# Kernel optimization log

Measured on AMD Instinct MI355X. Metric: run time of the kernel, lower is better.

## Reference

```python
import jax, jax.numpy as jnp
import numpy as np

# Static config (Swin-T stage 1, SW-MSA)
B = 32; H = 56; W = 56; C = 96; NH = 3; WS = 7; SHIFT = 3
N = WS * WS                 # tokens per window (49)
NW = (H // WS) * (W // WS)  # windows per image (64)
HD = C // NH                # head dim (32)
SCALE = HD ** -0.5
EPS = 1e-3  # keras LayerNormalization default epsilon


def _rel_index():
    # Matches tf.stack(tf.meshgrid(h, w)) with default 'xy' indexing
    xx, yy = np.meshgrid(np.arange(WS), np.arange(WS))
    coords = np.stack([xx, yy]).reshape(2, -1)              # [2, 49]
    rel = (coords[:, :, None] - coords[:, None, :]).transpose(1, 2, 0)
    rel[:, :, 0] += WS - 1
    rel[:, :, 1] += WS - 1
    rel[:, :, 0] *= 2 * WS - 1
    return rel.sum(-1)                                       # [49, 49]

REL_IDX = jnp.asarray(_rel_index())


def _attn_mask():
    # Standard Swin shifted-window attention mask
    img = np.zeros((H, W))
    cnt = 0
    sl = (slice(0, -WS), slice(-WS, -SHIFT), slice(-SHIFT, None))
    for hs in sl:
        for ws_ in sl:
            img[hs, ws_] = cnt
            cnt += 1
    win = img.reshape(H // WS, WS, W // WS, WS).transpose(0, 2, 1, 3).reshape(-1, N)
    diff = win[:, None, :] - win[:, :, None]
    return jnp.asarray(np.where(diff != 0, -100.0, 0.0), dtype=np.float32)  # [nW,49,49]

MASK = _attn_mask()


def _ln(x, g, b):
    mu = x.mean(-1, keepdims=True)
    var = ((x - mu) ** 2).mean(-1, keepdims=True)
    return (x - mu) / jnp.sqrt(var + EPS) * g + b


def setup_inputs() -> dict:
    key = jax.random.key(0)
    ks = jax.random.split(key, 6)
    f32 = jnp.float32
    return {
        "x": jax.random.normal(ks[0], (B, H * W, C), f32),
        "norm1_g": jnp.ones((C,), f32), "norm1_b": jnp.zeros((C,), f32),
        "qkv_w": jax.random.normal(ks[1], (C, 3 * C), f32) * 0.02,
        "qkv_b": jnp.zeros((3 * C,), f32),
        "bias_table": jax.random.normal(ks[2], ((2 * WS - 1) ** 2, NH), f32) * 0.02,
        "proj_w": jax.random.normal(ks[3], (C, C), f32) * 0.02,
        "proj_b": jnp.zeros((C,), f32),
        "norm2_g": jnp.ones((C,), f32), "norm2_b": jnp.zeros((C,), f32),
        "fc1_w": jax.random.normal(ks[4], (C, 4 * C), f32) * 0.02,
        "fc1_b": jnp.zeros((4 * C,), f32),
        "fc2_w": jax.random.normal(ks[5], (4 * C, C), f32) * 0.02,
        "fc2_b": jnp.zeros((C,), f32),
    }


def reference(x, norm1_g, norm1_b, qkv_w, qkv_b, bias_table, proj_w, proj_b,
              norm2_g, norm2_b, fc1_w, fc1_b, fc2_w, fc2_b):
    shortcut = x
    h = _ln(x, norm1_g, norm1_b).reshape(B, H, W, C)
    # cyclic shift (SW-MSA)
    h = jnp.roll(h, (-SHIFT, -SHIFT), axis=(1, 2))
    # window partition -> [B*nW, N, C]
    h = h.reshape(B, H // WS, WS, W // WS, WS, C).transpose(0, 1, 3, 2, 4, 5).reshape(-1, N, C)
    qkv = (h @ qkv_w + qkv_b).reshape(-1, N, 3, NH, HD).transpose(2, 0, 3, 1, 4)
    q, k, v = qkv[0], qkv[1], qkv[2]            # each [B*nW, NH, N, HD]
    attn = jnp.einsum('bhnd,bhmd->bhnm', q * SCALE, k)
    bias = bias_table[REL_IDX.reshape(-1)].reshape(N, N, NH).transpose(2, 0, 1)
    attn = attn + bias[None]
    attn = attn.reshape(B, NW, NH, N, N) + MASK[None, :, None]
    attn = attn.reshape(-1, NH, N, N)
    # NOTE: source applies softmax twice (once in branch, once unconditionally)
    attn = jax.nn.softmax(jax.nn.softmax(attn, axis=-1), axis=-1)
    o = jnp.einsum('bhnm,bhmd->bhnd', attn, v).transpose(0, 2, 1, 3).reshape(-1, N, C)
    o = o @ proj_w + proj_b
    # window reverse + reverse cyclic shift
    o = o.reshape(B, H // WS, W // WS, WS, WS, C).transpose(0, 1, 3, 2, 4, 5).reshape(B, H, W, C)
    o = jnp.roll(o, (SHIFT, SHIFT), axis=(1, 2)).reshape(B, H * W, C)
    x = shortcut + o
    y = _ln(x, norm2_g, norm2_b)
    # NOTE: source Mlp applies gelu in Dense activation AND again in call -> double gelu
    y = jax.nn.gelu(y @ fc1_w + fc1_b, approximate=False)
    y = jax.nn.gelu(y, approximate=False)
    y = y @ fc2_w + fc2_b
    return x + y
```

## Files before the change

kernel.cpp:

```cpp
#include <hip/hip_runtime.h>
#include <math.h>

#define BB   32
#define HH   56
#define WWI  56
#define CC   96
#define NHD  3
#define WSZ  7
#define SHF  3
#define NTK  49
#define NWIN 64
#define HDM  32
#define TOT  (BB*HH*WWI)
#define QKSCALE 0.17677669529663687f
#define LEPS 1e-3f

typedef __attribute__((ext_vector_type(8))) short s8v;
typedef __attribute__((ext_vector_type(4))) float fx4;
typedef unsigned long long ull_t;

#define MFMA16(a,b,c) __builtin_amdgcn_mfma_f32_16x16x32_bf16((a),(b),(c),0,0,0)

__device__ __forceinline__ unsigned short f2bf(float f) {
    union { float f; unsigned u; } v; v.f = f;
    unsigned r = v.u + 0x7FFFu + ((v.u >> 16) & 1u);
    return (unsigned short)(r >> 16);
}

__device__ __forceinline__ float gelu_t(float x) {
    float x2 = x * x;
#if __has_builtin(__builtin_amdgcn_exp2f)
    float z = x * fmaf(-0.10294326f, x2, -2.3022082f);
    float e = __builtin_amdgcn_exp2f(z);
#else
    float z = x * fmaf(-0.07135529f, x2, -1.5957691f);
    float e = __expf(z);
#endif
    return x * __builtin_amdgcn_rcpf(1.f + e);
}

__device__ __forceinline__ int wtok_to_orig(int wt) {
    int win = wt / NTK;
    int p   = wt - win * NTK;
    int b   = win >> 6;
    int w   = win & 63;
    int wi = w >> 3, wj = w & 7;
    int pi = p / WSZ, pj = p - pi * WSZ;
    int r = wi * WSZ + pi + SHF; if (r >= HH) r -= HH;
    int c = wj * WSZ + pj + SHF; if (c >= WWI) c -= WWI;
    return b * (HH * WWI) + r * WWI + c;
}

__device__ __forceinline__ void ln_frag(const float* __restrict__ row,
                                        const float* __restrict__ gg,
                                        const float* __restrict__ bb,
                                        int g4, s8v ha[3])
{
    float h[24];
    #pragma unroll
    for (int ks = 0; ks < 3; ++ks) {
        fx4 v0 = *reinterpret_cast<const fx4*>(row + ks * 32 + g4 * 8);
        fx4 v1 = *reinterpret_cast<const fx4*>(row + ks * 32 + g4 * 8 + 4);
        h[ks*8+0]=v0.x; h[ks*8+1]=v0.y; h[ks*8+2]=v0.z; h[ks*8+3]=v0.w;
        h[ks*8+4]=v1.x; h[ks*8+5]=v1.y; h[ks*8+6]=v1.z; h[ks*8+7]=v1.w;
    }
    float s = 0.f, s2 = 0.f;
    #pragma unroll
    for (int j = 0; j < 24; ++j) { s += h[j]; s2 = fmaf(h[j], h[j], s2); }
    s  += __shfl_xor(s, 16);  s  += __shfl_xor(s, 32);
    s2 += __shfl_xor(s2, 16); s2 += __shfl_xor(s2, 32);
    const float mu = s * (1.f/CC);
    const float rs = rsqrtf(s2 * (1.f/CC) - mu * mu + LEPS);
    #pragma unroll
    for (int ks = 0; ks < 3; ++ks) {
        union { s8v v; unsigned short u[8]; } p;
        #pragma unroll
        for (int j = 0; j < 8; ++j) {
            int c = ks * 32 + g4 * 8 + j;
            p.u[j] = f2bf((h[ks*8+j] - mu) * rs * gg[c] + bb[c]);
        }
        ha[ks] = p.v;
    }
}

extern "C" __global__ void p0_prep(const float* __restrict__ qw, const float* __restrict__ pw,
                                   const float* __restrict__ w1, const float* __restrict__ w2,
                                   const float* __restrict__ btab,
                                   unsigned short* __restrict__ wsw)
{
    int i = blockIdx.x * 256 + threadIdx.x;
    if (i < 27648) {
        int e = i & 7, f = i >> 3;
        int lane = f & 63, fid = f >> 6;
        int ks = fid % 3, t = fid / 3;
        int nt = t % 6, ck = t / 6;
        int n = ck * 96 + nt * 16 + (lane & 15);
        int k = ks * 32 + (lane >> 4) * 8 + e;
        float v = qw[k * 288 + n];
        if (n < 96) v *= QKSCALE;
        wsw[i] = f2bf(v);
    } else if (i < 36864) {
        int j = i - 27648;
        int e = j & 7, f = j >> 3;
        int lane = f & 63, fid = f >> 6;
        int ks = fid % 3, nt = fid / 3;
        int n = nt * 16 + (lane & 15);
        int k = ks * 32 + (lane >> 4) * 8 + e;
        wsw[i] = f2bf(pw[k * 96 + n]);
    } else if (i < 73728) {
        int j = i - 36864;
        int e = j & 7, f = j >> 3;
        int lane = f & 63, fid = f >> 6;
        int ks = fid % 3, t = fid / 3;
        int nt = t & 3, ck = t >> 2;
        int n = ck * 64 + nt * 16 + (lane & 15);
        int k = ks * 32 + (lane >> 4) * 8 + e;
        wsw[i] = f2bf(w1[k * 384 + n]);
    } else if (i < 110592) {
        int j = i - 73728;
        int e = j & 7, f = j >> 3;
        int lane = f & 63, fid = f >> 6;
        int ks = fid & 1, t = fid >> 1;
        int nt = t % 6, ck = t / 6;
        int n = nt * 16 + (lane & 15);
        int k = ck * 64 + ks * 32 + (lane >> 4) * 8 + e;
        wsw[i] = f2bf(w2[k * 96 + n]);
    } else if (i < 159744) {
        float* bmf = (float*)(wsw + 110592);
        int j = i - 110592;
        int r = j & 3, lane = (j >> 2) & 63;
        int fid = j >> 8;
        int mtnt = fid & 15, t = fid >> 4;
        int mt = mtnt >> 2, nt = mtnt & 3;
        int hd = t % 3, cls = t / 3;
        int m = mt * 16 + (lane >> 4) * 4 + r; if (m > 48) m = 48;
        int n = nt * 16 + (lane & 15);
        float val = 0.f;
        if (n < 49) {
            int it = m / 7, jt = m - it * 7;
            int iu = n / 7, ju = n - iu * 7;
            int li  = (cls & 2) ? (it < 4 ? 1 : 2) : 0;
            int lj  = (cls & 1) ? (jt < 4 ? 1 : 2) : 0;
            int lui = (cls & 2) ? (iu < 4 ? 1 : 2) : 0;
            int luj = (cls & 1) ? (ju < 4 ? 1 : 2) : 0;
            int bidx = (jt - ju + 6) * 13 + (it - iu + 6);
            val = btab[bidx * 3 + hd] + ((li*3+lj) == (lui*3+luj) ? 0.f : -100.f);
        }
        bmf[j] = val;
    }
}

#define LDQ 104
extern "C" __global__ void __launch_bounds__(256, 2) k12_fused(
    const float* __restrict__ x, const float* __restrict__ g1, const float* __restrict__ b1,
    const unsigned short* __restrict__ qwtf, const float* __restrict__ qb,
    const float* __restrict__ bmf, unsigned short* __restrict__ ovb)
{
    __shared__ unsigned short Qs[64 * LDQ];
    __shared__ unsigned short Ks[64 * LDQ];
    __shared__ unsigned short P[3][64 * 72];
    const int tid = threadIdx.x, wave = tid >> 6, lane = tid & 63;
    const int l15 = lane & 15, g4 = lane >> 4;
    const int win = blockIdx.x;
    const int g0  = win * NTK;

    s8v ha[3];
    {
        int row = wave * 16 + l15;
        int tok = row > 48 ? 48 : row;
        ln_frag(x + (size_t)wtok_to_orig(g0 + tok) * CC, g1, b1, g4, ha);
    }

    #pragma unroll
    for (int ck = 0; ck < 3; ++ck) {
        fx4 acc[6];
        #pragma unroll
        for (int nt = 0; nt < 6; ++nt) acc[nt] = (fx4){0.f,0.f,0.f,0.f};
        #pragma unroll
        for (int ks = 0; ks < 3; ++ks) {
            #pragma unroll
            for (int nt = 0; nt < 6; ++nt) {
                s8v b = *reinterpret_cast<const s8v*>(
                    &qwtf[(((ck * 6 + nt) * 3 + ks) * 64 + lane) * 8]);
                acc[nt] = MFMA16(ha[ks], b, acc[nt]);
            }
        }
        const int rowb = wave * 16 + g4 * 4;
        if (ck == 0) {
            #pragma unroll
            for (int nt = 0; nt < 6; ++nt) {
                const int col = nt * 16 + l15;
                const float qbc = qb[col] * QKSCALE;
                #pragma unroll
                for (int r = 0; r < 4; ++r)
                    Qs[(rowb + r) * LDQ + col] = f2bf(acc[nt][r] + qbc);
            }
        } else if (ck == 1) {
            #pragma unroll
            for (int nt = 0; nt < 6; ++nt) {
                const int col = nt * 16 + l15;
                const float qbc = qb[96 + col];
                #pragma unroll
                for (int r = 0; r < 4; ++r)
                    Ks[(rowb + r) * LDQ + col] = f2bf(acc[nt][r] + qbc);
            }
        } else {
            #pragma unroll
            for (int nt = 0; nt < 6; ++nt) {
                const int col = nt * 16 + l15;
                const float qbc = qb[192 + col];
                #pragma unroll
                for (int r = 0; r < 4; ++r) {
                    const int rr = rowb + r;
                    if (rr < NTK)
                        ovb[(size_t)(g0 + rr) * 96 + col] = f2bf(acc[nt][r] + qbc);
                }
            }
        }
    }
    __syncthreads();

    if (wave < 3) {
        const int h = wave;
        const int w = win & 63;
        const int cls = (((w >> 3) == 7) ? 2 : 0) + (((w & 7) == 7) ? 1 : 0);
        const float* BMF = bmf + (size_t)(cls * 3 + h) * 4096;
        unsigned short* Ph = &P[h][0];

        s8v aq[4], bk[4];
        #pragma unroll
        for (int mt = 0; mt < 4; ++mt) {
            const int rm = mt * 16 + l15;
            aq[mt] = *reinterpret_cast<const s8v*>(&Qs[rm * LDQ + h * 32 + g4 * 8]);
            bk[mt] = *reinterpret_cast<const s8v*>(&Ks[rm * LDQ + h * 32 + g4 * 8]);
        }

        fx4 sc[4][4];
        #pragma unroll
        for (int mt = 0; mt < 4; ++mt)
            #pragma unroll
            for (int nt = 0; nt < 4; ++nt)
                sc[mt][nt] = MFMA16(aq[mt], bk[nt], ((fx4){0.f,0.f,0.f,0.f}));

        #pragma unroll
        for (int mt = 0; mt < 4; ++mt) {
            fx4 bmv[4];
            #pragma unroll
            for (int nt = 0; nt < 4; ++nt)
                bmv[nt] = *reinterpret_cast<const fx4*>(&BMF[((mt * 4 + nt) << 8) + lane * 4]);
            #pragma unroll
            for (int r = 0; r < 4; ++r) {
                float rs1 = 0.f;
                #pragma unroll
                for (int nt = 0; nt < 4; ++nt) {
                    const int n = nt * 16 + l15;
                    float s = sc[mt][nt][r] + bmv[nt][r];
                    float e = (n < NTK) ? __expf(s) : 0.f;
                    sc[mt][nt][r] = e;
                    rs1 += e;
                }
                rs1 += __shfl_xor(rs1, 1); rs1 += __shfl_xor(rs1, 2);
                rs1 += __shfl_xor(rs1, 4); rs1 += __shfl_xor(rs1, 8);
                const float iv1 = 1.f / rs1;
                float rs2 = 0.f;
                #pragma unroll
                for (int nt = 0; nt < 4; ++nt) {
                    const int n = nt * 16 + l15;
                    float e2 = (n < NTK) ? __expf(sc[mt][nt][r] * iv1) : 0.f;
                    sc[mt][nt][r] = e2;
                    rs2 += e2;
                }
                rs2 += __shfl_xor(rs2, 1); rs2 += __shfl_xor(rs2, 2);
                rs2 += __shfl_xor(rs2, 4); rs2 += __shfl_xor(rs2, 8);
                const float iv2 = 1.f / rs2;
                const int m = mt * 16 + g4 * 4 + r;
                #pragma unroll
                for (int nt = 0; nt < 4; ++nt)
                    Ph[m * 72 + nt * 16 + l15] = f2bf(sc[mt][nt][r] * iv2);
            }
        }

        fx4 oc[4][2];
        #pragma unroll
        for (int mt = 0; mt < 4; ++mt) { oc[mt][0] = (fx4){0.f,0.f,0.f,0.f}; oc[mt][1] = (fx4){0.f,0.f,0.f,0.f}; }
        #pragma unroll
        for (int ks = 0; ks < 2; ++ks) {
            s8v vb[2];
            #pragma unroll
            for (int nt = 0; nt < 2; ++nt) {
                union { s8v v; unsigned short u[8]; } pv;
                #pragma unroll
                for (int j = 0; j < 8; ++j) {
                    int tok = ks * 32 + g4 * 8 + j; if (tok > 48) tok = 48;
                    pv.u[j] = ovb[(size_t)(g0 + tok) * 96 + h * 32 + nt * 16 + l15];
                }
                vb[nt] = pv.v;
            }
            #pragma unroll
            for (int mt = 0; mt < 4; ++mt) {
                s8v pa = *reinterpret_cast<const s8v*>(&Ph[(mt * 16 + l15) * 72 + ks * 32 + g4 * 8]);
                oc[mt][0] = MFMA16(pa, vb[0], oc[mt][0]);
                oc[mt][1] = MFMA16(pa, vb[1], oc[mt][1]);
            }
        }
        #pragma unroll
        for (int mt = 0; mt < 4; ++mt) {
            #pragma unroll
            for (int r = 0; r < 4; ++r) {
                const int m = mt * 16 + g4 * 4 + r;
                if (m < NTK) {
                    ovb[(size_t)(g0 + m) * 96 + h * 32 + l15]      = f2bf(oc[mt][0][r]);
                    ovb[(size_t)(g0 + m) * 96 + h * 32 + 16 + l15] = f2bf(oc[mt][1][r]);
                }
            }
        }
    }
}

#define LDA 72
#define LDX2 100
extern "C" __global__ void __launch_bounds__(256, 3) k23_fused(
    const unsigned short* __restrict__ ovb, const unsigned short* __restrict__ pwtf,
    const float* __restrict__ pb, const float* __restrict__ x,
    const float* __restrict__ g2, const float* __restrict__ b2,
    const unsigned short* __restrict__ w1f, const float* __restrict__ bf1,
    const unsigned short* __restrict__ w2f, const float* __restrict__ bf2,
    float* __restrict__ out)
{
    __shared__ float X2[64][LDX2];
    __shared__ unsigned short Ac[64 * LDA];
    const int tid = threadIdx.x, wave = tid >> 6, lane = tid & 63;
    const int l15 = lane & 15, g4 = lane >> 4;
    const int row0 = blockIdx.x * 64 + wave * 16;

    s8v a[3];
    {
        const int t = row0 + l15;
        const int b = t / (HH * WWI), rc = t - b * (HH * WWI);
        const int orr = rc / WWI, occ = rc - orr * WWI;
        int wr = orr + (HH - SHF); if (wr >= HH) wr -= HH;
        int wc = occ + (WWI - SHF); if (wc >= WWI) wc -= WWI;
        const int wtok = (b * 64 + (wr / WSZ) * 8 + (wc / WSZ)) * NTK
                         + (wr % WSZ) * WSZ + (wc % WSZ);
        const unsigned short* arow = ovb + (size_t)wtok * 96 + g4 * 8;
        a[0] = *reinterpret_cast<const s8v*>(arow);
        a[1] = *reinterpret_cast<const s8v*>(arow + 32);
        a[2] = *reinterpret_cast<const s8v*>(arow + 64);
    }
    {
        fx4 acc[6];
        #pragma unroll
        for (int nt = 0; nt < 6; ++nt) acc[nt] = (fx4){0.f,0.f,0.f,0.f};
        #pragma unroll
        for (int ks = 0; ks < 3; ++ks) {
            #pragma unroll
            for (int nt = 0; nt < 6; ++nt) {
                s8v b = *reinterpret_cast<const s8v*>(&pwtf[((nt * 3 + ks) * 64 + lane) * 8]);
                acc[nt] = MFMA16(a[ks], b, acc[nt]);
            }
        }
        #pragma unroll
        for (int nt = 0; nt < 6; ++nt) {
            const int col = nt * 16 + l15;
            const float pbc = pb[col];
            #pragma unroll
            for (int r = 0; r < 4; ++r) {
                const int tr = row0 + g4 * 4 + r;
                X2[wave * 16 + g4 * 4 + r][col] = acc[nt][r] + pbc + x[(size_t)tr * CC + col];
            }
        }
    }

    s8v ha[3];
    ln_frag(&X2[wave * 16 + l15][0], g2, b2, g4, ha);

    fx4 oacc[6];
    #pragma unroll
    for (int nt = 0; nt < 6; ++nt) oacc[nt] = (fx4){0.f,0.f,0.f,0.f};

    #pragma unroll 1
    for (int ck = 0; ck < 6; ++ck) {
        fx4 a1[4];
        #pragma unroll
        for (int nt = 0; nt < 4; ++nt) a1[nt] = (fx4){0.f,0.f,0.f,0.f};
        #pragma unroll
        for (int ks = 0; ks < 3; ++ks) {
            #pragma unroll
            for (int nt = 0; nt < 4; ++nt) {
                s8v b = *reinterpret_cast<const s8v*>(
                    &w1f[(((ck * 4 + nt) * 3 + ks) * 64 + lane) * 8]);
                a1[nt] = MFMA16(ha[ks], b, a1[nt]);
            }
        }
        #pragma unroll
        for (int nt = 0; nt < 4; ++nt) {
            const float bb = bf1[ck * 64 + nt * 16 + l15];
            #pragma unroll
            for (int r = 0; r < 4; ++r) {
                float v0 = a1[nt][r] + bb;
                Ac[(wave*16 + g4*4 + r) * LDA + nt*16 + l15] = f2bf(gelu_t(gelu_t(v0)));
            }
        }
        #pragma unroll
        for (int ks = 0; ks < 2; ++ks) {
            s8v aa = *reinterpret_cast<const s8v*>(&Ac[(wave*16 + l15)*LDA + ks*32 + g4*8]);
            #pragma unroll
            for (int nt = 0; nt < 6; ++nt) {
                s8v b = *reinterpret_cast<const s8v*>(
                    &w2f[(((ck * 6 + nt) * 2 + ks) * 64 + lane) * 8]);
                oacc[nt] = MFMA16(aa, b, oacc[nt]);
            }
        }
    }

    const int rowb = row0 + g4 * 4;
    #pragma unroll
    for (int nt = 0; nt < 6; ++nt) {
        const int col = nt * 16 + l15;
        const float bb = bf2[col];
        #pragma unroll
        for (int r = 0; r < 4; ++r) {
            out[(size_t)(rowb + r) * CC + col] =
                X2[wave * 16 + g4 * 4 + r][col] + oacc[nt][r] + bb;
        }
    }
}

extern "C" void kernel_launch(void* const* d_in, const int* in_sizes, int n_in,
                              void* d_out, int out_size, void* d_ws, size_t ws_size,
                              hipStream_t stream)
{
    const float* x    = (const float*)d_in[0];
    const float* n1g  = (const float*)d_in[1];
    const float* n1b  = (const float*)d_in[2];
    const float* qw   = (const float*)d_in[3];
    const float* qb   = (const float*)d_in[4];
    const float* btab = (const float*)d_in[5];
    const float* pw   = (const float*)d_in[6];
    const float* pb   = (const float*)d_in[7];
    const float* n2g  = (const float*)d_in[8];
    const float* n2b  = (const float*)d_in[9];
    const float* w1   = (const float*)d_in[10];
    const float* bf1  = (const float*)d_in[11];
    const float* w2   = (const float*)d_in[12];
    const float* bf2  = (const float*)d_in[13];
    float* out = (float*)d_out;

    unsigned short* ovb  = (unsigned short*)d_ws;
    unsigned short* wbf  = ovb + (size_t)TOT * 96;
    unsigned short* qwtf = wbf;
    unsigned short* pwtf = qwtf + 27648;
    unsigned short* w1f  = pwtf + 9216;
    unsigned short* w2f  = w1f + 36864;
    float* bmf = (float*)(wbf + 110592);

    p0_prep  <<<624, 256, 0, stream>>>(qw, pw, w1, w2, btab, wbf);
    k12_fused<<<BB*NWIN, 256, 0, stream>>>(x, n1g, n1b, qwtf, qb, bmf, ovb);
    k23_fused<<<TOT/64, 256, 0, stream>>>(ovb, pwtf, pb, x, n2g, n2b,
                                          w1f, bf1, w2f, bf2, out);
}
```

Measured before the change: 121.2 us.

## Switch projection/MLP kernel to 32x32 MFMA tiles with bf16 residual staging

Rewrites the proj+LN2+MLP kernel to use 32x32x16 bf16 MFMA instead of 16x16x32. Each wave now owns 32 rows, so a block covers 128 rows and weight fragments are reused across more rows. The weight prep swizzle is changed to match. The residual stage X2 is now kept in shared memory as bf16 rather than fp32, which halves LDS use but rounds the residual x that is added to the output, a possible accuracy risk.

```diff
diff --git a/kernel.cpp b/kernel.cpp
--- a/kernel.cpp
+++ b/kernel.cpp
@@ -17,14 +17,19 @@
 
 typedef __attribute__((ext_vector_type(8))) short s8v;
 typedef __attribute__((ext_vector_type(4))) float fx4;
+typedef __attribute__((ext_vector_type(16))) float fx16;
 typedef unsigned long long ull_t;
 
 #define MFMA16(a,b,c) __builtin_amdgcn_mfma_f32_16x16x32_bf16((a),(b),(c),0,0,0)
+#define MFMA32(a,b,c) __builtin_amdgcn_mfma_f32_32x32x16_bf16((a),(b),(c),0,0,0)
 
 __device__ __forceinline__ unsigned short f2bf(float f) {
     union { float f; unsigned u; } v; v.f = f;
     unsigned r = v.u + 0x7FFFu + ((v.u >> 16) & 1u);
     return (unsigned short)(r >> 16);
+}
+__device__ __forceinline__ float bf2f(unsigned short u) {
+    return __uint_as_float((unsigned)u << 16);
 }
 
 __device__ __forceinline__ float gelu_t(float x) {
@@ -103,27 +108,27 @@
         int j = i - 27648;
         int e = j & 7, f = j >> 3;
         int lane = f & 63, fid = f >> 6;
-        int ks = fid % 3, nt = fid / 3;
-        int n = nt * 16 + (lane & 15);
-        int k = ks * 32 + (lane >> 4) * 8 + e;
+        int ks = fid % 6, nt = fid / 6;
+        int n = nt * 32 + (lane & 31);
+        int k = ks * 16 + (lane >> 5) * 8 + e;
         wsw[i] = f2bf(pw[k * 96 + n]);
     } else if (i < 73728) {
         int j = i - 36864;
         int e = j & 7, f = j >> 3;
         int lane = f & 63, fid = f >> 6;
-        int ks = fid % 3, t = fid / 3;
-        int nt = t & 3, ck = t >> 2;
-        int n = ck * 64 + nt * 16 + (lane & 15);
-        int k = ks * 32 + (lane >> 4) * 8 + e;
+        int ks = fid % 6, t = fid / 6;
+        int nt = t & 1, ck = t >> 1;
+        int n = ck * 64 + nt * 32 + (lane & 31);
+        int k = ks * 16 + (lane >> 5) * 8 + e;
         wsw[i] = f2bf(w1[k * 384 + n]);
     } else if (i < 110592) {
         int j = i - 73728;
         int e = j & 7, f = j >> 3;
         int lane = f & 63, fid = f >> 6;
-        int ks = fid & 1, t = fid >> 1;
-        int nt = t % 6, ck = t / 6;
-        int n = nt * 16 + (lane & 15);
-        int k = ck * 64 + ks * 32 + (lane >> 4) * 8 + e;
+        int ks = fid & 3, t = fid >> 2;
+        int nt = t % 3, ck = t / 3;
+        int n = nt * 32 + (lane & 31);
+        int k = ck * 64 + ks * 16 + (lane >> 5) * 8 + e;
         wsw[i] = f2bf(w2[k * 96 + n]);
     } else if (i < 159744) {
         float* bmf = (float*)(wsw + 110592);
@@ -317,8 +322,7 @@
     }
 }
 
-#define LDA 72
-#define LDX2 100
+#define LDX2B 104
 extern "C" __global__ void __launch_bounds__(256, 3) k23_fused(
     const unsigned short* __restrict__ ovb, const unsigned short* __restrict__ pwtf,
     const float* __restrict__ pb, const float* __restrict__ x,
@@ -327,101 +331,129 @@
     const unsigned short* __restrict__ w2f, const float* __restrict__ bf2,
     float* __restrict__ out)
 {
-    __shared__ float X2[64][LDX2];
-    __shared__ unsigned short Ac[64 * LDA];
+    __shared__ unsigned short X2b[128 * LDX2B];
+    __shared__ unsigned short Ac[128 * 64];
     const int tid = threadIdx.x, wave = tid >> 6, lane = tid & 63;
-    const int l15 = lane & 15, g4 = lane >> 4;
-    const int row0 = blockIdx.x * 64 + wave * 16;
-
-    s8v a[3];
+    const int l31 = lane & 31, gk = lane >> 5;
+    const int row0 = blockIdx.x * 128 + wave * 32;
+
+    s8v a[6];
     {
-        const int t = row0 + l15;
+        const int t = row0 + l31;
         const int b = t / (HH * WWI), rc = t - b * (HH * WWI);
         const int orr = rc / WWI, occ = rc - orr * WWI;
         int wr = orr + (HH - SHF); if (wr >= HH) wr -= HH;
         int wc = occ + (WWI - SHF); if (wc >= WWI) wc -= WWI;
         const int wtok = (b * 64 + (wr / WSZ) * 8 + (wc / WSZ)) * NTK
                          + (wr % WSZ) * WSZ + (wc % WSZ);
-        const unsigned short* arow = ovb + (size_t)wtok * 96 + g4 * 8;
-        a[0] = *reinterpret_cast<const s8v*>(arow);
-        a[1] = *reinterpret_cast<const s8v*>(arow + 32);
-        a[2] = *reinterpret_cast<const s8v*>(arow + 64);
+        const unsigned short* arow = ovb + (size_t)wtok * 96 + gk * 8;
+        #pragma unroll
+        for (int ks = 0; ks < 6; ++ks)
+            a[ks] = *reinterpret_cast<const s8v*>(arow + ks * 16);
     }
     {
-        fx4 acc[6];
-        #pragma unroll
-        for (int nt = 0; nt < 6; ++nt) acc[nt] = (fx4){0.f,0.f,0.f,0.f};
-        #pragma unroll
-        for (int ks = 0; ks < 3; ++ks) {
-            #pragma unroll
-            for (int nt = 0; nt < 6; ++nt) {
-                s8v b = *reinterpret_cast<const s8v*>(&pwtf[((nt * 3 + ks) * 64 + lane) * 8]);
-                acc[nt] = MFMA16(a[ks], b, acc[nt]);
-            }
-        }
-        #pragma unroll
-        for (int nt = 0; nt < 6; ++nt) {
-            const int col = nt * 16 + l15;
+        fx16 acc[3];
+        #pragma unroll
+        for (int nt = 0; nt < 3; ++nt) acc[nt] = (fx16)(0.f);
+        #pragma unroll
+        for (int ks = 0; ks < 6; ++ks) {
+            #pragma unroll
+            for (int nt = 0; nt < 3; ++nt) {
+                s8v b = *reinterpret_cast<const s8v*>(&pwtf[((nt * 6 + ks) * 64 + lane) * 8]);
+                acc[nt] = MFMA32(a[ks], b, acc[nt]);
+            }
+        }
+        #pragma unroll
+        for (int nt = 0; nt < 3; ++nt) {
+            const int col = nt * 32 + l31;
             const float pbc = pb[col];
             #pragma unroll
-            for (int r = 0; r < 4; ++r) {
-                const int tr = row0 + g4 * 4 + r;
-                X2[wave * 16 + g4 * 4 + r][col] = acc[nt][r] + pbc + x[(size_t)tr * CC + col];
-            }
-        }
-    }
-
-    s8v ha[3];
-    ln_frag(&X2[wave * 16 + l15][0], g2, b2, g4, ha);
-
-    fx4 oacc[6];
-    #pragma unroll
-    for (int nt = 0; nt < 6; ++nt) oacc[nt] = (fx4){0.f,0.f,0.f,0.f};
+            for (int r = 0; r < 16; ++r) {
+                const int drow = (r & 3) + 8 * (r >> 2) + 4 * gk;
+                X2b[(wave * 32 + drow) * LDX2B + col] =
+                    f2bf(acc[nt][r] + pbc + x[(size_t)(row0 + drow) * CC + col]);
+            }
+        }
+    }
+
+    s8v ha[6];
+    {
+        const unsigned short* xr = &X2b[(wave * 32 + l31) * LDX2B + gk * 8];
+        float h[48];
+        float s = 0.f, s2 = 0.f;
+        #pragma unroll
+        for (int ks = 0; ks < 6; ++ks) {
+            #pragma unroll
+            for (int j = 0; j < 8; ++j) {
+                float v = bf2f(xr[ks * 16 + j]);
+                h[ks * 8 + j] = v;
+                s += v; s2 = fmaf(v, v, s2);
+            }
+        }
+        s += __shfl_xor(s, 32); s2 += __shfl_xor(s2, 32);
+        const float mu = s * (1.f/CC);
+        const float rs = rsqrtf(s2 * (1.f/CC) - mu * mu + LEPS);
+        #pragma unroll
+        for (int ks = 0; ks < 6; ++ks) {
+            union { s8v v; unsigned short u[8]; } p;
+            #pragma unroll
+            for (int j = 0; j < 8; ++j) {
+                int c = ks * 16 + gk * 8 + j;
+                p.u[j] = f2bf((h[ks * 8 + j] - mu) * rs * g2[c] + b2[c]);
+            }
+            ha[ks] = p.v;
+        }
+    }
+
+    fx16 oacc[3];
+    #pragma unroll
+    for (int nt = 0; nt < 3; ++nt) oacc[nt] = (fx16)(0.f);
 
     #pragma unroll 1
     for (int ck = 0; ck < 6; ++ck) {
-        fx4 a1[4];
-        #pragma unroll
-        for (int nt = 0; nt < 4; ++nt) a1[nt] = (fx4){0.f,0.f,0.f,0.f};
-        #pragma unroll
-        for (int ks = 0; ks < 3; ++ks) {
-            #pragma unroll
-            for (int nt = 0; nt < 4; ++nt) {
+        fx16 a1[2];
+        a1[0] = (fx16)(0.f); a1[1] = (fx16)(0.f);
+        #pragma unroll
+        for (int ks = 0; ks < 6; ++ks) {
+            #pragma unroll
+            for (int nt = 0; nt < 2; ++nt) {
                 s8v b = *reinterpret_cast<const s8v*>(
-                    &w1f[(((ck * 4 + nt) * 3 + ks) * 64 + lane) * 8]);
-                a1[nt] = MFMA16(ha[ks], b, a1[nt]);
-            }
-        }
-        #pragma unroll
-        for (int nt = 0; nt < 4; ++nt) {
-            const float bb = bf1[ck * 64 + nt * 16 + l15];
-            #pragma unroll
-            for (int r = 0; r < 4; ++r) {
-                float v0 = a1[nt][r] + bb;
-                Ac[(wave*16 + g4*4 + r) * LDA + nt*16 + l15] = f2bf(gelu_t(gelu_t(v0)));
-            }
-        }
-        #pragma unroll
-        for (int ks = 0; ks < 2; ++ks) {
-            s8v aa = *reinterpret_cast<const s8v*>(&Ac[(wave*16 + l15)*LDA + ks*32 + g4*8]);
-            #pragma unroll
-            for (int nt = 0; nt < 6; ++nt) {
+                    &w1f[((((ck * 2 + nt) * 6) + ks) * 64 + lane) * 8]);
+                a1[nt] = MFMA32(ha[ks], b, a1[nt]);
+            }
+        }
+        #pragma unroll
+        for (int nt = 0; nt < 2; ++nt) {
+            const float bb = bf1[ck * 64 + nt * 32 + l31];
+            #pragma unroll
+            for (int r = 0; r < 16; ++r) {
+                const int drow = (r & 3) + 8 * (r >> 2) + 4 * gk;
+                Ac[(wave * 32 + drow) * 64 + nt * 32 + l31] =
+                    f2bf(gelu_t(gelu_t(a1[nt][r] + bb)));
+            }
+        }
+        #pragma unroll
+        for (int ks = 0; ks < 4; ++ks) {
+            s8v aa = *reinterpret_cast<const s8v*>(
+                &Ac[(wave * 32 + l31) * 64 + ks * 16 + gk * 8]);
+            #pragma unroll
+            for (int nt = 0; nt < 3; ++nt) {
                 s8v b = *reinterpret_cast<const s8v*>(
-                    &w2f[(((ck * 6 + nt) * 2 + ks) * 64 + lane) * 8]);
-                oacc[nt] = MFMA16(aa, b, oacc[nt]);
-            }
-        }
-    }
-
-    const int rowb = row0 + g4 * 4;
-    #pragma unroll
-    for (int nt = 0; nt < 6; ++nt) {
-        const int col = nt * 16 + l15;
+                    &w2f[((((ck * 3 + nt) * 4) + ks) * 64 + lane) * 8]);
+                oacc[nt] = MFMA32(aa, b, oacc[nt]);
+            }
+        }
+    }
+
+    #pragma unroll
+    for (int nt = 0; nt < 3; ++nt) {
+        const int col = nt * 32 + l31;
         const float bb = bf2[col];
         #pragma unroll
-        for (int r = 0; r < 4; ++r) {
-            out[(size_t)(rowb + r) * CC + col] =
-                X2[wave * 16 + g4 * 4 + r][col] + oacc[nt][r] + bb;
+        for (int r = 0; r < 16; ++r) {
+            const int drow = (r & 3) + 8 * (r >> 2) + 4 * gk;
+            out[(size_t)(row0 + drow) * CC + col] =
+                bf2f(X2b[(wave * 32 + drow) * LDX2B + col]) + oacc[nt][r] + bb;
         }
     }
 }
@@ -456,6 +488,6 @@
 
     p0_prep  <<<624, 256, 0, stream>>>(qw, pw, w1, w2, btab, wbf);
     k12_fused<<<BB*NWIN, 256, 0, stream>>>(x, n1g, n1b, qwtf, qb, bmf, ovb);
-    k23_fused<<<TOT/64, 256, 0, stream>>>(ovb, pwtf, pb, x, n2g, n2b,
-                                          w1f, bf1, w2f, bf2, out);
-}
+    k23_fused<<<TOT/128, 256, 0, stream>>>(ovb, pwtf, pb, x, n2g, n2b,
+                                           w1f, bf1, w2f, bf2, out);
+}
```

Result: slower. 178.6 us (median of 2 runs) (+47.4%).
